# Kernel optimization log

Hardware: AMD Instinct MI355X
Metric: run time of the kernel (lower is better)

Reference implementation:

```python
import jax, jax.numpy as jnp
import numpy as np

L, DIM, S = 4, 17, 4
B, H, W = 4, 256, 256
BINSIZE = 16.0


def setup_inputs() -> dict:
    key = jax.random.key(0)
    k1, k2, k3, k4 = jax.random.split(key, 4)
    lut = jax.random.normal(k1, (L, DIM, DIM, DIM, DIM, S, S), dtype=jnp.float32)
    tri_index = jax.random.normal(k2, (24, 4), dtype=jnp.float32)
    weight = jax.random.uniform(k3, (B, L, H, W), dtype=jnp.float32)
    x = jax.random.uniform(k4, (B, 1, H, W), dtype=jnp.float32) * 255.0
    return {"lut": lut, "tri_index": tri_index, "weight": weight, "x": x, "scale_factor": S}


def _quadrilinear(lut, weight, x, s):
    # lut: [L, D, D, D, D, s, s]; weight: [B, L, H, W]; x: [B, 1, H, W] in [0,255]
    Bx, C, Hx, Wx = x.shape
    Lx, D = lut.shape[0], lut.shape[1]
    # reflection pad right/bottom by 1, take the 2x2 neighborhood -> 4 LUT coords
    xp = jnp.pad(x, ((0, 0), (0, 0), (0, 1), (0, 1)), mode="reflect")
    pix = jnp.stack([xp[:, :, :Hx, :Wx], xp[:, :, :Hx, 1:Wx + 1],
                     xp[:, :, 1:Hx + 1, :Wx], xp[:, :, 1:Hx + 1, 1:Wx + 1]], axis=-1)  # [B,C,H,W,4]
    t = pix / BINSIZE
    base_f = jnp.floor(t)
    frac = t - base_f                                   # [B,C,H,W,4] in [0,1)
    base = jnp.clip(base_f, 0, D - 2).astype(jnp.int32)  # [B,C,H,W,4]
    # 4D simplex (generalized tetrahedral) interpolation: sort fracs descending
    order = jnp.argsort(-frac, axis=-1)                 # [B,C,H,W,4]
    sf = jnp.take_along_axis(frac, order, axis=-1)      # sorted desc
    wts = jnp.stack([1.0 - sf[..., 0],
                     sf[..., 0] - sf[..., 1],
                     sf[..., 1] - sf[..., 2],
                     sf[..., 2] - sf[..., 3],
                     sf[..., 3]], axis=-1)              # [B,C,H,W,5]
    oneh = jax.nn.one_hot(order, 4, dtype=jnp.int32)    # [B,C,H,W,4,4]
    cum = jnp.cumsum(oneh, axis=-2)                     # vertex k offset = sum of top-k one-hots
    offs = jnp.concatenate([jnp.zeros_like(cum[..., :1, :]), cum], axis=-2)  # [B,C,H,W,5,4]
    vidx = base[..., None, :] + offs                    # [B,C,H,W,5,4]
    flat = ((vidx[..., 0] * D + vidx[..., 1]) * D + vidx[..., 2]) * D + vidx[..., 3]  # [B,C,H,W,5]
    lut_flat = lut.reshape(Lx, D ** 4, s * s)
    gathered = lut_flat[:, flat]                        # [L,B,C,H,W,5,s*s]
    interp = jnp.einsum("lbchwks,bchwk->lbchws", gathered, wts)  # [L,B,C,H,W,s*s]
    out = jnp.einsum("lbchws,blhw->bchws", interp, weight)       # [B,C,H,W,s*s]
    out = out.reshape(Bx, C, Hx, Wx, s, s).transpose(0, 1, 2, 4, 3, 5)
    return out.reshape(Bx, C, Hx * s, Wx * s)


def reference(lut, tri_index, weight, x, scale_factor):
    # tri_index encodes the precomputed simplex permutation table used by the CUDA
    # kernel; the reference derives the permutation analytically (argsort), so it is unused.
    return _quadrilinear(lut, weight, x, int(scale_factor))
```

## Files before the change

kernel.cpp:

```cpp
#include <hip/hip_runtime.h>
#include <hip/hip_fp16.h>

#define HH   256
#define WW   256
#define HWPX (HH * WW)
#define DD   17
#define D4   (17 * 17 * 17 * 17)
#define NL   4
#define SS   16
#define LUT_FLOATS  (NL * D4 * SS)
#define LUT_BYTES_H ((size_t)LUT_FLOATS * 2)

__global__ __launch_bounds__(256) void lut_transpose_h_kernel(
    const float4* __restrict__ src,
    ushort* __restrict__ dst)
{
    int t = blockIdx.x * blockDim.x + threadIdx.x;
    if (t >= D4 * NL * 4) return;
    int c4 = t & 3;
    int l  = (t >> 2) & 3;
    int v  = t >> 4;
    float4 r = src[(size_t)l * (D4 * 4) + (size_t)v * 4 + c4];
    ushort4 h;
    h.x = __half_as_ushort(__float2half_rn(r.x));
    h.y = __half_as_ushort(__float2half_rn(r.y));
    h.z = __half_as_ushort(__float2half_rn(r.z));
    h.w = __half_as_ushort(__float2half_rn(r.w));
    *((ushort4*)(dst + (size_t)t * 4)) = h;
}

__global__ __launch_bounds__(256) void lut4d_kernel_v(
    const ushort* __restrict__ lutT,
    const float* __restrict__ weight,
    const float* __restrict__ x,
    float* __restrict__ out)
{
    int tid = blockIdx.x * blockDim.x + threadIdx.x;
    int j = tid & 7;
    int p = tid >> 3;
    int b  = p >> 16;
    int hw = p & 65535;
    int h  = hw >> 8;
    int w  = hw & 255;
    int l  = j >> 1;

    const float* xb = x + b * HWPX;
    int h1 = (h + 1 < HH) ? (h + 1) : (HH - 2);
    int w1 = (w + 1 < WW) ? (w + 1) : (WW - 2);

    float pix0 = xb[h  * WW + w ];
    float pix1 = xb[h  * WW + w1];
    float pix2 = xb[h1 * WW + w ];
    float pix3 = xb[h1 * WW + w1];

    float wlv = weight[(size_t)b * (NL * HWPX) + (size_t)l * HWPX + hw];

    const float inv = 1.0f / 16.0f;
    float t0 = pix0 * inv, t1 = pix1 * inv, t2 = pix2 * inv, t3 = pix3 * inv;
    float bf0 = floorf(t0), bf1 = floorf(t1), bf2 = floorf(t2), bf3 = floorf(t3);
    float f0 = t0 - bf0, f1 = t1 - bf1, f2 = t2 - bf2, f3 = t3 - bf3;

    int b0 = min(max((int)bf0, 0), DD - 2);
    int b1 = min(max((int)bf1, 0), DD - 2);
    int b2 = min(max((int)bf2, 0), DD - 2);
    int b3 = min(max((int)bf3, 0), DD - 2);

    float s0f = f0, s1f = f1, s2f = f2, s3f = f3;
    int   s0s = 4913, s1s = 289, s2s = 17, s3s = 1;

#define CSWAP(fa, sa, fb, sb)                                          \
    do {                                                               \
        bool sw = (fb > fa) || ((fb == fa) && (sb > sa));              \
        float tf = fa; int ts = sa;                                    \
        if (sw) { fa = fb; sa = sb; fb = tf; sb = ts; }                \
    } while (0)

    CSWAP(s0f, s0s, s1f, s1s);
    CSWAP(s2f, s2s, s3f, s3s);
    CSWAP(s0f, s0s, s2f, s2s);
    CSWAP(s1f, s1s, s3f, s3s);
    CSWAP(s1f, s1s, s2f, s2s);
#undef CSWAP

    float wts[5];
    wts[0] = 1.0f - s0f;
    wts[1] = s0f - s1f;
    wts[2] = s1f - s2f;
    wts[3] = s2f - s3f;
    wts[4] = s3f;

    int flats[5];
    flats[0] = ((b0 * DD + b1) * DD + b2) * DD + b3;
    flats[1] = flats[0] + s0s;
    flats[2] = flats[1] + s1s;
    flats[3] = flats[2] + s2s;
    flats[4] = flats[3] + s3s;

    uint4 r[5];
#pragma unroll
    for (int k = 0; k < 5; ++k) {
        const ushort* vbase = lutT + (size_t)flats[k] * (NL * SS);
        r[k] = *((const uint4*)(vbase) + j);
    }

    float acc0 = 0.f, acc1 = 0.f, acc2 = 0.f, acc3 = 0.f;
    float acc4 = 0.f, acc5 = 0.f, acc6 = 0.f, acc7 = 0.f;
#pragma unroll
    for (int k = 0; k < 5; ++k) {
        float c = wlv * wts[k];
        float2 f0v = __half22float2(*reinterpret_cast<const __half2*>(&r[k].x));
        float2 f1v = __half22float2(*reinterpret_cast<const __half2*>(&r[k].y));
        float2 f2v = __half22float2(*reinterpret_cast<const __half2*>(&r[k].z));
        float2 f3v = __half22float2(*reinterpret_cast<const __half2*>(&r[k].w));
        acc0 = fmaf(c, f0v.x, acc0);
        acc1 = fmaf(c, f0v.y, acc1);
        acc2 = fmaf(c, f1v.x, acc2);
        acc3 = fmaf(c, f1v.y, acc3);
        acc4 = fmaf(c, f2v.x, acc4);
        acc5 = fmaf(c, f2v.y, acc5);
        acc6 = fmaf(c, f3v.x, acc6);
        acc7 = fmaf(c, f3v.y, acc7);
    }

#define RED(mask)                                                      \
    do {                                                               \
        acc0 += __shfl_xor(acc0, mask, 64);                            \
        acc1 += __shfl_xor(acc1, mask, 64);                            \
        acc2 += __shfl_xor(acc2, mask, 64);                            \
        acc3 += __shfl_xor(acc3, mask, 64);                            \
        acc4 += __shfl_xor(acc4, mask, 64);                            \
        acc5 += __shfl_xor(acc5, mask, 64);                            \
        acc6 += __shfl_xor(acc6, mask, 64);                            \
        acc7 += __shfl_xor(acc7, mask, 64);                            \
    } while (0)
    RED(2);
    RED(4);
#undef RED

    int sel = j >> 1;
    float o0 = (sel == 0) ? acc0 : (sel == 1) ? acc2 : (sel == 2) ? acc4 : acc6;
    float o1 = (sel == 0) ? acc1 : (sel == 1) ? acc3 : (sel == 2) ? acc5 : acc7;

    int c0  = (j & 1) * 8 + sel * 2;
    int row = c0 >> 2;
    int col = c0 & 3;
    float* ob = out + (size_t)b * (HH * 4) * (WW * 4)
                    + (size_t)(h * 4 + row) * (WW * 4)
                    + (w * 4) + col;
    *((float2*)ob) = make_float2(o0, o1);
}

__global__ __launch_bounds__(256) void lut4d_kernel_fallback(
    const float* __restrict__ lut,
    const float* __restrict__ weight,
    const float* __restrict__ x,
    float* __restrict__ out)
{
    int p = blockIdx.x * blockDim.x + threadIdx.x;
    int b  = p >> 16;
    int hw = p & 65535;
    int h  = hw >> 8;
    int w  = hw & 255;

    const float* xb = x + b * HWPX;
    int h1 = (h + 1 < HH) ? (h + 1) : (HH - 2);
    int w1 = (w + 1 < WW) ? (w + 1) : (WW - 2);

    float pix0 = xb[h  * WW + w ];
    float pix1 = xb[h  * WW + w1];
    float pix2 = xb[h1 * WW + w ];
    float pix3 = xb[h1 * WW + w1];

    const float inv = 1.0f / 16.0f;
    float t0 = pix0 * inv, t1 = pix1 * inv, t2 = pix2 * inv, t3 = pix3 * inv;
    float bf0 = floorf(t0), bf1 = floorf(t1), bf2 = floorf(t2), bf3 = floorf(t3);
    float f0 = t0 - bf0, f1 = t1 - bf1, f2 = t2 - bf2, f3 = t3 - bf3;

    int b0 = min(max((int)bf0, 0), DD - 2);
    int b1 = min(max((int)bf1, 0), DD - 2);
    int b2 = min(max((int)bf2, 0), DD - 2);
    int b3 = min(max((int)bf3, 0), DD - 2);

    float s0f = f0, s1f = f1, s2f = f2, s3f = f3;
    int   s0s = 4913, s1s = 289, s2s = 17, s3s = 1;

#define CSWAP(fa, sa, fb, sb)                                          \
    do {                                                               \
        bool sw = (fb > fa) || ((fb == fa) && (sb > sa));              \
        float tf = fa; int ts = sa;                                    \
        if (sw) { fa = fb; sa = sb; fb = tf; sb = ts; }                \
    } while (0)

    CSWAP(s0f, s0s, s1f, s1s);
    CSWAP(s2f, s2s, s3f, s3s);
    CSWAP(s0f, s0s, s2f, s2s);
    CSWAP(s1f, s1s, s3f, s3s);
    CSWAP(s1f, s1s, s2f, s2s);
#undef CSWAP

    float wts[5] = { 1.0f - s0f, s0f - s1f, s1f - s2f, s2f - s3f, s3f };
    int flats[5];
    flats[0] = ((b0 * DD + b1) * DD + b2) * DD + b3;
    flats[1] = flats[0] + s0s;
    flats[2] = flats[1] + s1s;
    flats[3] = flats[2] + s2s;
    flats[4] = flats[3] + s3s;

    float acc[SS];
#pragma unroll
    for (int i = 0; i < SS; ++i) acc[i] = 0.0f;

    const float* wb = weight + b * (NL * HWPX) + hw;

#pragma unroll
    for (int l = 0; l < NL; ++l) {
        float wlv = wb[l * HWPX];
        const float* lbase = lut + (size_t)l * D4 * SS;
#pragma unroll
        for (int k = 0; k < 5; ++k) {
            float c = wlv * wts[k];
            const float4* row = (const float4*)(lbase + (size_t)flats[k] * SS);
#pragma unroll
            for (int q = 0; q < 4; ++q) {
                float4 rr = row[q];
                acc[q * 4 + 0] = fmaf(c, rr.x, acc[q * 4 + 0]);
                acc[q * 4 + 1] = fmaf(c, rr.y, acc[q * 4 + 1]);
                acc[q * 4 + 2] = fmaf(c, rr.z, acc[q * 4 + 2]);
                acc[q * 4 + 3] = fmaf(c, rr.w, acc[q * 4 + 3]);
            }
        }
    }

    float* ob = out + (size_t)b * (HH * 4) * (WW * 4) + (size_t)(h * 4) * (WW * 4) + (w * 4);
#pragma unroll
    for (int i = 0; i < 4; ++i) {
        *((float4*)(ob + (size_t)i * (WW * 4))) =
            make_float4(acc[i * 4 + 0], acc[i * 4 + 1], acc[i * 4 + 2], acc[i * 4 + 3]);
    }
}

extern "C" void kernel_launch(void* const* d_in, const int* in_sizes, int n_in,
                              void* d_out, int out_size, void* d_ws, size_t ws_size,
                              hipStream_t stream) {
    const float* lut    = (const float*)d_in[0];
    const float* weight = (const float*)d_in[2];
    const float* x      = (const float*)d_in[3];
    float* out          = (float*)d_out;

    dim3 block(256);

    if (ws_size >= LUT_BYTES_H) {
        ushort* lutT = (ushort*)d_ws;
        int n_chunks = D4 * NL * 4;
        dim3 grid_t((n_chunks + 255) / 256);
        hipLaunchKernelGGL(lut_transpose_h_kernel, grid_t, block, 0, stream,
                           (const float4*)lut, lutT);
        dim3 grid_main(8192);
        hipLaunchKernelGGL(lut4d_kernel_v, grid_main, block, 0, stream,
                           lutT, weight, x, out);
    } else {
        dim3 grid_main(1024);
        hipLaunchKernelGGL(lut4d_kernel_fallback, grid_main, block, 0, stream,
                           lut, weight, x, out);
    }
}
```

Baseline: 99.80 us.

## Bucket-sort pixels by LUT base index before gathering for locality

Adds a histogram, scan and scatter pass that counting-sorts pixels into coarse bins of their base LUT index, staging the per-pixel layer weights in sorted order. The main kernel then walks pixels in sorted order and remaps blocks across bins, so concurrent waves gather nearby LUT rows and reuse cache. This adds four extra launches, global atomics and scattered output writes in exchange for better gather locality on the large fp16 LUT.

```diff
diff --git a/kernel.cpp b/kernel.cpp
--- a/kernel.cpp
+++ b/kernel.cpp
@@ -8,8 +8,49 @@
 #define D4   (17 * 17 * 17 * 17)
 #define NL   4
 #define SS   16
+#define NPIX (4 * HWPX)
 #define LUT_FLOATS  (NL * D4 * SS)
 #define LUT_BYTES_H ((size_t)LUT_FLOATS * 2)
+
+#define NBINS     160
+#define BIN_SHIFT 9
+
+#define WSO_HIST    0u
+#define WSO_CURSOR  1024u
+#define WSO_SORTP   (1u << 20)
+#define WSO_WA      (4u << 20)
+#define WSO_WB      (8u << 20)
+#define WSO_LUT     (12u << 20)
+#define WS_NEED     ((size_t)WSO_LUT + LUT_BYTES_H)
+
+__device__ __forceinline__ void pixel_base(
+    const float* __restrict__ x, int p,
+    int& b, int& hw,
+    int& bq0, int& bq1, int& bq2, int& bq3,
+    float& f0, float& f1, float& f2, float& f3)
+{
+    b  = p >> 16;
+    hw = p & 65535;
+    int h = hw >> 8, w = hw & 255;
+    const float* xb = x + b * HWPX;
+    int h1 = (h + 1 < HH) ? (h + 1) : (HH - 2);
+    int w1 = (w + 1 < WW) ? (w + 1) : (WW - 2);
+
+    float pix0 = xb[h  * WW + w ];
+    float pix1 = xb[h  * WW + w1];
+    float pix2 = xb[h1 * WW + w ];
+    float pix3 = xb[h1 * WW + w1];
+
+    const float inv = 1.0f / 16.0f;
+    float t0 = pix0 * inv, t1 = pix1 * inv, t2 = pix2 * inv, t3 = pix3 * inv;
+    float bf0 = floorf(t0), bf1 = floorf(t1), bf2 = floorf(t2), bf3 = floorf(t3);
+    f0 = t0 - bf0; f1 = t1 - bf1; f2 = t2 - bf2; f3 = t3 - bf3;
+
+    bq0 = min(max((int)bf0, 0), DD - 2);
+    bq1 = min(max((int)bf1, 0), DD - 2);
+    bq2 = min(max((int)bf2, 0), DD - 2);
+    bq3 = min(max((int)bf3, 0), DD - 2);
+}
 
 __global__ __launch_bounds__(256) void lut_transpose_h_kernel(
     const float4* __restrict__ src,
@@ -29,50 +70,103 @@
     *((ushort4*)(dst + (size_t)t * 4)) = h;
 }
 
-__global__ __launch_bounds__(256) void lut4d_kernel_v(
+__global__ __launch_bounds__(256) void lut4d_zero_meta(unsigned* __restrict__ ws)
+{
+    int t = threadIdx.x;
+    ws[t]       = 0;
+    ws[256 + t] = 0;
+}
+
+__global__ __launch_bounds__(256) void lut4d_hist(
+    const float* __restrict__ x, unsigned* __restrict__ hist)
+{
+    __shared__ unsigned lh[NBINS];
+    int t = threadIdx.x;
+    if (t < NBINS) lh[t] = 0;
+    __syncthreads();
+
+    int p = blockIdx.x * 256 + t;
+    int b, hw, b0, b1, b2, b3; float f0, f1, f2, f3;
+    pixel_base(x, p, b, hw, b0, b1, b2, b3, f0, f1, f2, f3);
+    int flat0 = ((b0 * DD + b1) * DD + b2) * DD + b3;
+    atomicAdd(&lh[flat0 >> BIN_SHIFT], 1u);
+    __syncthreads();
+
+    if (t < NBINS) {
+        unsigned c = lh[t];
+        if (c) atomicAdd(&hist[t], c);
+    }
+}
+
+__global__ __launch_bounds__(256) void lut4d_scan(
+    const unsigned* __restrict__ hist, unsigned* __restrict__ cursor)
+{
+    __shared__ unsigned sdat[256];
+    int t = threadIdx.x;
+    unsigned v = (t < NBINS) ? hist[t] : 0u;
+    sdat[t] = v;
+    __syncthreads();
+#pragma unroll
+    for (int off = 1; off < 256; off <<= 1) {
+        unsigned a = (t >= off) ? sdat[t - off] : 0u;
+        __syncthreads();
+        sdat[t] += a;
+        __syncthreads();
+    }
+    if (t < NBINS) cursor[t] = sdat[t] - v;
+}
+
+__global__ __launch_bounds__(256) void lut4d_scatter(
+    const float* __restrict__ x, const float* __restrict__ weight,
+    unsigned* __restrict__ cursor,
+    unsigned* __restrict__ sortP, float2* __restrict__ wA, float2* __restrict__ wB)
+{
+    int p = blockIdx.x * 256 + threadIdx.x;
+    int b, hw, b0, b1, b2, b3; float f0, f1, f2, f3;
+    pixel_base(x, p, b, hw, b0, b1, b2, b3, f0, f1, f2, f3);
+    int flat0 = ((b0 * DD + b1) * DD + b2) * DD + b3;
+    int bin = flat0 >> BIN_SHIFT;
+
+    const float* wb = weight + b * (NL * HWPX) + hw;
+    float wl0 = wb[0 * HWPX], wl1 = wb[1 * HWPX];
+    float wl2 = wb[2 * HWPX], wl3 = wb[3 * HWPX];
+
+    unsigned pos = atomicAdd(&cursor[bin], 1u);
+    sortP[pos] = (unsigned)p;
+    wA[pos] = make_float2(wl0, wl1);
+    wB[pos] = make_float2(wl2, wl3);
+}
+
+__global__ __launch_bounds__(256) void lut4d_main_sorted(
     const ushort* __restrict__ lutT,
-    const float* __restrict__ weight,
+    const unsigned* __restrict__ sortP,
+    const float2* __restrict__ wA, const float2* __restrict__ wB,
     const float* __restrict__ x,
     float* __restrict__ out)
 {
-    int tid = blockIdx.x * blockDim.x + threadIdx.x;
-    int j = tid & 7;
-    int p = tid >> 3;
-    int b  = p >> 16;
-    int hw = p & 65535;
-    int h  = hw >> 8;
-    int w  = hw & 255;
-    int l  = j >> 1;
-
-    const float* xb = x + b * HWPX;
-    int h1 = (h + 1 < HH) ? (h + 1) : (HH - 2);
-    int w1 = (w + 1 < WW) ? (w + 1) : (WW - 2);
-
-    float pix0 = xb[h  * WW + w ];
-    float pix1 = xb[h  * WW + w1];
-    float pix2 = xb[h1 * WW + w ];
-    float pix3 = xb[h1 * WW + w1];
-
-    float wlv = weight[(size_t)b * (NL * HWPX) + (size_t)l * HWPX + hw];
-
-    const float inv = 1.0f / 16.0f;
-    float t0 = pix0 * inv, t1 = pix1 * inv, t2 = pix2 * inv, t3 = pix3 * inv;
-    float bf0 = floorf(t0), bf1 = floorf(t1), bf2 = floorf(t2), bf3 = floorf(t3);
-    float f0 = t0 - bf0, f1 = t1 - bf1, f2 = t2 - bf2, f3 = t3 - bf3;
-
-    int b0 = min(max((int)bf0, 0), DD - 2);
-    int b1 = min(max((int)bf1, 0), DD - 2);
-    int b2 = min(max((int)bf2, 0), DD - 2);
-    int b3 = min(max((int)bf3, 0), DD - 2);
+    int c = (blockIdx.x & 7) * 1024 + (blockIdx.x >> 3);
+    int t = threadIdx.x;
+    int j = t & 7;
+    int sidx = c * 32 + (t >> 3);
+    int l = j >> 1;
+
+    int p = (int)sortP[sidx];
+    float2 fa = wA[sidx];
+    float2 fb = wB[sidx];
+    float wlv = (l == 0) ? fa.x : (l == 1) ? fa.y : (l == 2) ? fb.x : fb.y;
+
+    int b, hw, b0, b1, b2, b3; float f0, f1, f2, f3;
+    pixel_base(x, p, b, hw, b0, b1, b2, b3, f0, f1, f2, f3);
+    int h = hw >> 8, w = hw & 255;
 
     float s0f = f0, s1f = f1, s2f = f2, s3f = f3;
     int   s0s = 4913, s1s = 289, s2s = 17, s3s = 1;
 
-#define CSWAP(fa, sa, fb, sb)                                          \
+#define CSWAP(fa_, sa_, fb_, sb_)                                      \
     do {                                                               \
-        bool sw = (fb > fa) || ((fb == fa) && (sb > sa));              \
-        float tf = fa; int ts = sa;                                    \
-        if (sw) { fa = fb; sa = sb; fb = tf; sb = ts; }                \
+        bool sw = (fb_ > fa_) || ((fb_ == fa_) && (sb_ > sa_));        \
+        float tf = fa_; int ts = sa_;                                  \
+        if (sw) { fa_ = fb_; sa_ = sb_; fb_ = tf; sb_ = ts; }          \
     } while (0)
 
     CSWAP(s0f, s0s, s1f, s1s);
@@ -107,19 +201,19 @@
     float acc4 = 0.f, acc5 = 0.f, acc6 = 0.f, acc7 = 0.f;
 #pragma unroll
     for (int k = 0; k < 5; ++k) {
-        float c = wlv * wts[k];
+        float cw = wlv * wts[k];
         float2 f0v = __half22float2(*reinterpret_cast<const __half2*>(&r[k].x));
         float2 f1v = __half22float2(*reinterpret_cast<const __half2*>(&r[k].y));
         float2 f2v = __half22float2(*reinterpret_cast<const __half2*>(&r[k].z));
         float2 f3v = __half22float2(*reinterpret_cast<const __half2*>(&r[k].w));
-        acc0 = fmaf(c, f0v.x, acc0);
-        acc1 = fmaf(c, f0v.y, acc1);
-        acc2 = fmaf(c, f1v.x, acc2);
-        acc3 = fmaf(c, f1v.y, acc3);
-        acc4 = fmaf(c, f2v.x, acc4);
-        acc5 = fmaf(c, f2v.y, acc5);
-        acc6 = fmaf(c, f3v.x, acc6);
-        acc7 = fmaf(c, f3v.y, acc7);
+        acc0 = fmaf(cw, f0v.x, acc0);
+        acc1 = fmaf(cw, f0v.y, acc1);
+        acc2 = fmaf(cw, f1v.x, acc2);
+        acc3 = fmaf(cw, f1v.y, acc3);
+        acc4 = fmaf(cw, f2v.x, acc4);
+        acc5 = fmaf(cw, f2v.y, acc5);
+        acc6 = fmaf(cw, f3v.x, acc6);
+        acc7 = fmaf(cw, f3v.y, acc7);
     }
 
 #define RED(mask)                                                      \
@@ -157,38 +251,18 @@
     float* __restrict__ out)
 {
     int p = blockIdx.x * blockDim.x + threadIdx.x;
-    int b  = p >> 16;
-    int hw = p & 65535;
-    int h  = hw >> 8;
-    int w  = hw & 255;
-
-    const float* xb = x + b * HWPX;
-    int h1 = (h + 1 < HH) ? (h + 1) : (HH - 2);
-    int w1 = (w + 1 < WW) ? (w + 1) : (WW - 2);
-
-    float pix0 = xb[h  * WW + w ];
-    float pix1 = xb[h  * WW + w1];
-    float pix2 = xb[h1 * WW + w ];
-    float pix3 = xb[h1 * WW + w1];
-
-    const float inv = 1.0f / 16.0f;
-    float t0 = pix0 * inv, t1 = pix1 * inv, t2 = pix2 * inv, t3 = pix3 * inv;
-    float bf0 = floorf(t0), bf1 = floorf(t1), bf2 = floorf(t2), bf3 = floorf(t3);
-    float f0 = t0 - bf0, f1 = t1 - bf1, f2 = t2 - bf2, f3 = t3 - bf3;
-
-    int b0 = min(max((int)bf0, 0), DD - 2);
-    int b1 = min(max((int)bf1, 0), DD - 2);
-    int b2 = min(max((int)bf2, 0), DD - 2);
-    int b3 = min(max((int)bf3, 0), DD - 2);
+    int b, hw, b0, b1, b2, b3; float f0, f1, f2, f3;
+    pixel_base(x, p, b, hw, b0, b1, b2, b3, f0, f1, f2, f3);
+    int h = hw >> 8, w = hw & 255;
 
     float s0f = f0, s1f = f1, s2f = f2, s3f = f3;
     int   s0s = 4913, s1s = 289, s2s = 17, s3s = 1;
 
-#define CSWAP(fa, sa, fb, sb)                                          \
+#define CSWAP(fa_, sa_, fb_, sb_)                                      \
     do {                                                               \
-        bool sw = (fb > fa) || ((fb == fa) && (sb > sa));              \
-        float tf = fa; int ts = sa;                                    \
-        if (sw) { fa = fb; sa = sb; fb = tf; sb = ts; }                \
+        bool sw = (fb_ > fa_) || ((fb_ == fa_) && (sb_ > sa_));        \
+        float tf = fa_; int ts = sa_;                                  \
+        if (sw) { fa_ = fb_; sa_ = sb_; fb_ = tf; sb_ = ts; }          \
     } while (0)
 
     CSWAP(s0f, s0s, s1f, s1s);
@@ -218,15 +292,15 @@
         const float* lbase = lut + (size_t)l * D4 * SS;
 #pragma unroll
         for (int k = 0; k < 5; ++k) {
-            float c = wlv * wts[k];
+            float cw = wlv * wts[k];
             const float4* row = (const float4*)(lbase + (size_t)flats[k] * SS);
 #pragma unroll
             for (int q = 0; q < 4; ++q) {
                 float4 rr = row[q];
-                acc[q * 4 + 0] = fmaf(c, rr.x, acc[q * 4 + 0]);
-                acc[q * 4 + 1] = fmaf(c, rr.y, acc[q * 4 + 1]);
-                acc[q * 4 + 2] = fmaf(c, rr.z, acc[q * 4 + 2]);
-                acc[q * 4 + 3] = fmaf(c, rr.w, acc[q * 4 + 3]);
+                acc[q * 4 + 0] = fmaf(cw, rr.x, acc[q * 4 + 0]);
+                acc[q * 4 + 1] = fmaf(cw, rr.y, acc[q * 4 + 1]);
+                acc[q * 4 + 2] = fmaf(cw, rr.z, acc[q * 4 + 2]);
+                acc[q * 4 + 3] = fmaf(cw, rr.w, acc[q * 4 + 3]);
             }
         }
     }
@@ -249,15 +323,29 @@
 
     dim3 block(256);
 
-    if (ws_size >= LUT_BYTES_H) {
-        ushort* lutT = (ushort*)d_ws;
+    if (ws_size >= WS_NEED) {
+        char* ws = (char*)d_ws;
+        unsigned* hist   = (unsigned*)(ws + WSO_HIST);
+        unsigned* cursor = (unsigned*)(ws + WSO_CURSOR);
+        unsigned* sortP  = (unsigned*)(ws + WSO_SORTP);
+        float2*   wA     = (float2*)  (ws + WSO_WA);
+        float2*   wB     = (float2*)  (ws + WSO_WB);
+        ushort*   lutT   = (ushort*)  (ws + WSO_LUT);
+
         int n_chunks = D4 * NL * 4;
         dim3 grid_t((n_chunks + 255) / 256);
         hipLaunchKernelGGL(lut_transpose_h_kernel, grid_t, block, 0, stream,
                            (const float4*)lut, lutT);
-        dim3 grid_main(8192);
-        hipLaunchKernelGGL(lut4d_kernel_v, grid_main, block, 0, stream,
-                           lutT, weight, x, out);
+        hipLaunchKernelGGL(lut4d_zero_meta, dim3(1), block, 0, stream,
+                           (unsigned*)ws);
+        hipLaunchKernelGGL(lut4d_hist, dim3(NPIX / 256), block, 0, stream,
+                           x, hist);
+        hipLaunchKernelGGL(lut4d_scan, dim3(1), block, 0, stream,
+                           hist, cursor);
+        hipLaunchKernelGGL(lut4d_scatter, dim3(NPIX / 256), block, 0, stream,
+                           x, weight, cursor, sortP, wA, wB);
+        hipLaunchKernelGGL(lut4d_main_sorted, dim3(8192), block, 0, stream,
+                           lutT, sortP, wA, wB, x, out);
     } else {
         dim3 grid_main(1024);
         hipLaunchKernelGGL(lut4d_kernel_fallback, grid_main, block, 0, stream,
```

Result: slower. 310.3 us (+211.0%).
